# Optimization experiments

Hardware: AMD Instinct MI355X
Metric: run time of the kernel (lower is better)

## Reference

```python
import jax, jax.numpy as jnp
import numpy as np

B, N, C_IN = 4, 4096, 64
DIM = 64
NKP = 15
K = 32               # neighbor_limits
CONV_RADIUS = 0.1 * 2.0   # conv_radius * rigid_scale (is_deform=False)
KERNEL_RADIUS = 0.12
RECEP = 1.2          # kernel_point_receptive_radius
TRANS_DIM = 128
INF = 1000000.0


def _square_distance(src, dst):
    # src [B,N,3], dst [B,M,3] -> [B,N,M]
    d = -2.0 * jnp.einsum('bnc,bmc->bnm', src, dst)
    d = d + jnp.sum(src * src, -1)[:, :, None]
    d = d + jnp.sum(dst * dst, -1)[:, None, :]
    return d


def _query_ball(xyz, radius):
    # xyz [B,N,3] -> neighbor idx [B,N,K]; out-of-radius mapped to N (shadow)
    n = xyz.shape[1]
    sq = _square_distance(xyz, xyz)
    idx = jnp.broadcast_to(jnp.arange(n, dtype=jnp.int32), sq.shape)
    idx = jnp.where(sq > radius * radius, n, idx)
    idx = jnp.sort(idx, axis=-1)[:, :, :K]
    return idx


def _index_points(points_bcn, idx, pad_val):
    # points [B,C,N], idx [B,N,K] -> [B,N,K,C]; index N hits shadow row = pad_val
    p = jnp.transpose(points_bcn, (0, 2, 1))          # [B,N,C]
    shadow = jnp.full((p.shape[0], 1, p.shape[2]), pad_val, p.dtype)
    p = jnp.concatenate([p, shadow], axis=1)          # [B,N+1,C]
    b_idx = jnp.arange(p.shape[0])[:, None, None]
    return p[b_idx, idx]                              # [B,N,K,C]


def setup_inputs() -> dict:
    key = jax.random.key(0)
    ks = jax.random.split(key, 12)
    pos = jax.random.uniform(ks[0], (B, 3, N), dtype=jnp.float32)
    feat = jax.random.normal(ks[1], (B, C_IN, N), dtype=jnp.float32)
    # kernel points: center point at origin, rest inside kernel_radius ball ('center' mode)
    kp_rest = jax.random.uniform(ks[2], (3, NKP - 1), minval=-KERNEL_RADIUS,
                                 maxval=KERNEL_RADIUS, dtype=jnp.float32)
    kp_pos = jnp.concatenate([jnp.zeros((3, 1), jnp.float32), kp_rest], axis=1)  # [3,NKP]
    s = 0.05
    cb_w = jax.random.normal(ks[3], (DIM, C_IN), jnp.float32) * s
    cb_b = jax.random.normal(ks[4], (DIM,), jnp.float32) * s
    kp_weight = jax.random.normal(ks[5], (NKP, DIM, DIM), jnp.float32) * s
    kp_bias = jax.random.normal(ks[6], (DIM,), jnp.float32) * s
    ce_w = jax.random.normal(ks[7], (C_IN, DIM), jnp.float32) * s
    ce_b = jax.random.normal(ks[8], (C_IN,), jnp.float32) * s
    f1_w = jax.random.normal(ks[9], (2 * DIM, 2 * DIM), jnp.float32) * s
    f1_b = jnp.zeros((2 * DIM,), jnp.float32)
    f2_w = jax.random.normal(ks[10], (TRANS_DIM, 2 * DIM), jnp.float32) * s
    f2_b = jnp.zeros((TRANS_DIM,), jnp.float32)
    return dict(pos=pos, feat=feat, kp_pos=kp_pos, cb_w=cb_w, cb_b=cb_b,
                kp_weight=kp_weight, kp_bias=kp_bias, ce_w=ce_w, ce_b=ce_b,
                f1_w=f1_w, f1_b=f1_b, f2_w=f2_w, f2_b=f2_b)


def reference(pos, feat, kp_pos, cb_w, cb_b, kp_weight, kp_bias, ce_w, ce_b,
              f1_w, f1_b, f2_w, f2_b):
    xyz = jnp.transpose(jax.lax.stop_gradient(pos), (0, 2, 1))       # [B,N,3]
    neighbor_idx = _query_ball(xyz, CONV_RADIUS)                     # [B,N,K]
    # NOTE: with is_deform=False the original code does NOT subtract the center
    # position; rel_neighbor_pos is the absolute gathered positions.
    neighbor_pos = jnp.transpose(_index_points(pos, neighbor_idx, INF),
                                 (0, 3, 1, 2))                        # [B,3,N,K]
    feat0 = jnp.einsum('oc,bcn->bon', cb_w, feat) + cb_b[None, :, None]
    neighbor_feat = _index_points(feat0, neighbor_idx, 0.0)           # [B,N,K,DIM]

    kp_pos_deform = kp_pos.reshape(1, 3, 1, NKP) + 0.0                # offset = 0
    diff = neighbor_pos[..., None] - kp_pos_deform[:, :, :, None, :]  # [B,3,N,K,NKP]
    sq_d = jnp.sum(diff * diff, axis=1)                               # [B,N,K,NKP]
    w = jnp.clip(1.0 - jnp.sqrt(sq_d) / RECEP, 0.0)                   # [B,N,K,NKP]
    w = jnp.transpose(w, (0, 1, 3, 2))                                # [B,N,NKP,K]
    weighted = jnp.einsum('bnpk,bnkc->bnpc', w, neighbor_feat)        # [B,N,NKP,DIM]
    out = jnp.einsum('bnpc,pcd->bnd', weighted, kp_weight) + kp_bias  # [B,N,DIM]
    out = jax.nn.relu(jnp.transpose(out, (0, 2, 1)))                  # [B,DIM,N]
    out = jax.nn.relu(jnp.einsum('oc,bcn->bon', ce_w, out)
                      + ce_b[None, :, None] + feat)                   # [B,C_IN,N]

    fuse_in = jnp.concatenate(
        [jnp.transpose(weighted, (0, 3, 1, 2)),                       # [B,DIM,N,NKP]
         jnp.broadcast_to(out[..., None], (B, DIM, N, NKP))], axis=1) # [B,2DIM,N,NKP]
    h = jax.nn.relu(jnp.einsum('oc,bcnk->bonk', f1_w, fuse_in)
                    + f1_b[None, :, None, None])
    fuse = jax.nn.relu(jnp.einsum('oc,bcnk->bonk', f2_w, h)
                       + f2_b[None, :, None, None])                   # [B,TRANS_DIM,N,NKP]
    return out, kp_pos_deform, fuse
```

## Files before the change

kernel.cpp:

```cpp
#include <hip/hip_runtime.h>
#include <hip/hip_bf16.h>
#include <stdint.h>

#define NPTS 4096
#define NB   4
#define KNN  32
#define NKPT 15

#define OFF_IDX      0ULL
#define OFF_FEAT0    2097152ULL
#define OFF_WEIGHTED 6292480ULL
#define OFF_HO       37749760ULL
#define OFF_W1P      46138368ULL
#define OFF_W2P      46171136ULL
#define OFF_KPWP     46203904ULL

#define OUT_OFF_OUT  0
#define OUT_OFF_KP   1048576
#define OUT_OFF_FUSE 1048621

#define SBU(u) ((u) ^ (((u) >> 3) & 7))

typedef __attribute__((ext_vector_type(8))) short short8v;
typedef __attribute__((ext_vector_type(4))) float f32x4;

__device__ __forceinline__ unsigned short bf16b(float f) {
  __hip_bfloat16 h = __float2bfloat16(f);
  return *(unsigned short*)&h;
}
__device__ __forceinline__ unsigned pkbf(float lo, float hi) {
  return (unsigned)bf16b(lo) | ((unsigned)bf16b(hi) << 16);
}

__global__ __launch_bounds__(256) void k012(const float* __restrict__ pos,
                                            const float* __restrict__ feat,
                                            const float* __restrict__ cb_w,
                                            const float* __restrict__ cb_b,
                                            const float* __restrict__ f1_w,
                                            const float* __restrict__ f2_w,
                                            const float* __restrict__ kpw,
                                            const float* __restrict__ kp_pos,
                                            int* __restrict__ idx_ws,
                                            float* __restrict__ feat0,
                                            unsigned short* __restrict__ w1p,
                                            unsigned short* __restrict__ w2p,
                                            unsigned short* __restrict__ kpwp,
                                            float* __restrict__ out_kp) {
  __shared__ float cbt[64 * 65];
  const int blk = blockIdx.x;
  if (blk < 4096) {
    const int w = threadIdx.x >> 6, lane = threadIdx.x & 63;
    const int pt = blk * 4 + w;
    const int b = pt >> 12, n = pt & 4095;
    const float* px = pos + (size_t)b * 3 * NPTS;
    const double x0 = (double)px[n], y0 = (double)px[NPTS + n], z0 = (double)px[2 * NPTS + n];
    const double ssrc = x0 * x0 + y0 * y0 + z0 * z0;
    const double RAD = 0.1 * 2.0;
    const double R2 = RAD * RAD;
    int cnt = 0;
    int* op = idx_ws + (size_t)pt * KNN;
    for (int ch = 0; ch < 64; ++ch) {
      const int j = ch * 64 + lane;
      const double xj = (double)px[j], yj = (double)px[NPTS + j], zj = (double)px[2 * NPTS + j];
      const double dot  = x0 * xj + y0 * yj + z0 * zj;
      const double sdst = xj * xj + yj * yj + zj * zj;
      const double sq = -2.0 * dot + ssrc + sdst;
      const bool keep = !(sq > R2);
      const unsigned long long m = __ballot(keep);
      if (keep) {
        const int p = cnt + (int)__popcll(m & ((1ULL << lane) - 1ULL));
        if (p < KNN) op[p] = j;
      }
      cnt += (int)__popcll(m);
      if (cnt >= KNN) break;
    }
    const int s = cnt + lane;
    if (s < KNN) op[s] = NPTS;
    return;
  }
  if (blk < 8192) {
    const int t = threadIdx.x;
    #pragma unroll
    for (int q = 0; q < 16; ++q) {
      const int idx = q * 256 + t;
      const int d = idx >> 6, c = idx & 63;
      cbt[c * 65 + d] = cb_w[idx];
    }
    __syncthreads();
    const int ptl = t >> 6, d = t & 63;
    const int pt = (blk - 4096) * 4 + ptl;
    const int b = pt >> 12, n = pt & 4095;
    const float* fp = feat + (size_t)b * 64 * NPTS + n;
    float acc = 0.f;
    #pragma unroll
    for (int c = 0; c < 64; ++c) acc = fmaf(cbt[c * 65 + d], fp[(size_t)c * NPTS], acc);
    acc += cb_b[d];
    feat0[((size_t)b * (NPTS + 1) + n) * 64 + d] = acc;
    return;
  }
  int t = (blk - 8192) * 256 + threadIdx.x;
  if (t < 32768) {
    const int w = t >> 14;
    const int i = t & 16383;
    const int j = i & 7, l = (i >> 3) & 63, kc = (i >> 9) & 3, ot = i >> 11;
    const int o = ot * 16 + (l & 15);
    const int k = kc * 32 + (l >> 4) * 8 + j;
    const float* src = w ? f2_w : f1_w;
    unsigned short* dst = w ? w2p : w1p;
    dst[i] = bf16b(src[o * 128 + k]);
    return;
  }
  t -= 32768;
  if (t < 61440) {
    const int j = t & 7, l = (t >> 3) & 63, nt = (t >> 9) & 3, kc = t >> 11;
    const int k = kc * 32 + (l >> 4) * 8 + j;
    const int d = nt * 16 + (l & 15);
    kpwp[t] = bf16b(kpw[(size_t)k * 64 + d]);
    return;
  }
  t -= 61440;
  if (t < NB * 64) { int b = t >> 6, d = t & 63; feat0[((size_t)b * (NPTS + 1) + NPTS) * 64 + d] = 0.f; return; }
  t -= NB * 64;
  if (t < 45) out_kp[t] = kp_pos[t];
}

__global__ __launch_bounds__(64) void k3_weighted(const float* __restrict__ pos,
                                                  const int* __restrict__ idx_ws,
                                                  const float* __restrict__ feat0,
                                                  const float* __restrict__ kp_pos,
                                                  unsigned short* __restrict__ wbf) {
  __shared__ int   nidx[KNN];
  __shared__ float npx[KNN], npy[KNN], npz[KNN];
  __shared__ float kp[48];
  __shared__ float wl[KNN * 16];
  const int lane = threadIdx.x;
  const int pt = blockIdx.x;
  const int b = pt >> 12;
  if (lane < 45) kp[lane] = kp_pos[lane];
  if (lane < KNN) {
    const int ki = idx_ws[(size_t)pt * KNN + lane];
    nidx[lane] = ki;
    const bool v = ki < NPTS;
    const float* px = pos + (size_t)b * 3 * NPTS;
    npx[lane] = v ? px[ki] : 1000000.0f;
    npy[lane] = v ? px[NPTS + ki] : 1000000.0f;
    npz[lane] = v ? px[2 * NPTS + ki] : 1000000.0f;
  }
  __syncthreads();
  #pragma unroll
  for (int r = 0; r < 8; ++r) {
    const int i = r * 64 + lane;
    const int k = i >> 4, p = i & 15;
    float wv = 0.f;
    if (p < 15) {
      const float dx = npx[k] - kp[p];
      const float dy = npy[k] - kp[15 + p];
      const float dz = npz[k] - kp[30 + p];
      const float d2 = dx * dx + dy * dy + dz * dz;
      wv = fmaxf(1.0f - sqrtf(d2) / 1.2f, 0.f);
    }
    wl[i] = wv;
  }
  __syncthreads();
  float acc[16];
  #pragma unroll
  for (int p = 0; p < 16; ++p) acc[p] = 0.f;
  const float* f0 = feat0 + (size_t)b * (NPTS + 1) * 64 + lane;
  for (int k = 0; k < KNN; ++k) {
    const float f = f0[(size_t)nidx[k] * 64];
    #pragma unroll
    for (int q = 0; q < 4; ++q) {
      const float4 w4 = *(const float4*)&wl[k * 16 + q * 4];
      acc[q * 4 + 0] = fmaf(w4.x, f, acc[q * 4 + 0]);
      acc[q * 4 + 1] = fmaf(w4.y, f, acc[q * 4 + 1]);
      acc[q * 4 + 2] = fmaf(w4.z, f, acc[q * 4 + 2]);
      acc[q * 4 + 3] = fmaf(w4.w, f, acc[q * 4 + 3]);
    }
  }
  unsigned short* wp = wbf + (size_t)pt * NKPT * 64 + lane;
  #pragma unroll
  for (int p = 0; p < 15; ++p) wp[(size_t)p * 64] = bf16b(acc[p]);
}

__global__ __launch_bounds__(256) void k45(const unsigned short* __restrict__ wbf,
                                           const unsigned short* __restrict__ kpwp,
                                           const float* __restrict__ kp_bias,
                                           const float* __restrict__ ce_w,
                                           const float* __restrict__ ce_b,
                                           const float* __restrict__ feat,
                                           const unsigned short* __restrict__ w1p,
                                           const float* __restrict__ f1_b,
                                           float* __restrict__ out,
                                           float* __restrict__ hO) {
  __shared__ float r0[64 * 65];
  __shared__ float cwt[64 * 64];
  __shared__ unsigned short outT[64 * 74];
  const int t = threadIdx.x;
  const int b = blockIdx.x >> 6;
  const int n0 = (blockIdx.x & 63) * 64;
  const int wv = t >> 6, lane = t & 63;
  #pragma unroll
  for (int q = 0; q < 16; ++q) {
    const int idx = q * 256 + t;
    cwt[idx] = ce_w[(idx & 63) * 64 + (idx >> 6)];
  }
  const short8v* kf = (const short8v*)kpwp;
  f32x4 acc[4];
  #pragma unroll
  for (int nt = 0; nt < 4; ++nt) acc[nt] = (f32x4){0.f, 0.f, 0.f, 0.f};
  const int m0 = b * 4096 + n0 + wv * 16;
  const unsigned short* ap = wbf + (size_t)(m0 + (lane & 15)) * 960 + (lane >> 4) * 8;
  #pragma unroll 6
  for (int kc = 0; kc < 30; ++kc) {
    const short8v a = *(const short8v*)&ap[kc * 32];
    #pragma unroll
    for (int nt = 0; nt < 4; ++nt)
      acc[nt] = __builtin_amdgcn_mfma_f32_16x16x32_bf16(a, kf[(kc * 4 + nt) * 64 + lane], acc[nt], 0, 0, 0);
  }
  const int rl = wv * 16 + (lane >> 4) * 4;
  #pragma unroll
  for (int nt = 0; nt < 4; ++nt) {
    const int d = nt * 16 + (lane & 15);
    const float bv = kp_bias[d];
    #pragma unroll
    for (int r = 0; r < 4; ++r)
      r0[(rl + r) * 65 + d] = fmaxf(acc[nt][r] + bv, 0.f);
  }
  __syncthreads();
  const int nl = t & 63, og = t >> 6;
  float facc[16];
  #pragma unroll
  for (int j = 0; j < 16; ++j) facc[j] = 0.f;
  for (int c = 0; c < 64; ++c) {
    const float x = r0[nl * 65 + c];
    #pragma unroll
    for (int q = 0; q < 4; ++q) {
      const float4 w4 = *(const float4*)&cwt[c * 64 + og * 16 + q * 4];
      facc[q * 4 + 0] = fmaf(w4.x, x, facc[q * 4 + 0]);
      facc[q * 4 + 1] = fmaf(w4.y, x, facc[q * 4 + 1]);
      facc[q * 4 + 2] = fmaf(w4.z, x, facc[q * 4 + 2]);
      facc[q * 4 + 3] = fmaf(w4.w, x, facc[q * 4 + 3]);
    }
  }
  #pragma unroll
  for (int q = 0; q < 4; ++q) {
    const float4 cb4 = *(const float4*)&ce_b[og * 16 + q * 4];
    const float cbv[4] = {cb4.x, cb4.y, cb4.z, cb4.w};
    #pragma unroll
    for (int j = 0; j < 4; ++j) {
      const int o = og * 16 + q * 4 + j;
      const float fv = feat[((size_t)b * 64 + o) * 4096 + n0 + nl];
      const float v = fmaxf((facc[q * 4 + j] + cbv[j]) + fv, 0.f);
      out[((size_t)b * 64 + o) * 4096 + n0 + nl] = v;
      outT[o * 74 + nl] = bf16b(v);
    }
  }
  __syncthreads();
  const short8v* w1f = (const short8v*)w1p;
  f32x4 hacc[8];
  #pragma unroll
  for (int ot = 0; ot < 8; ++ot) hacc[ot] = (f32x4){0.f, 0.f, 0.f, 0.f};
  const int nw = lane & 15;
  #pragma unroll
  for (int kc2 = 0; kc2 < 2; ++kc2) {
    short8v bfr;
    #pragma unroll
    for (int j = 0; j < 8; ++j)
      bfr[j] = (short)outT[(kc2 * 32 + (lane >> 4) * 8 + j) * 74 + wv * 16 + nw];
    #pragma unroll
    for (int ot = 0; ot < 8; ++ot)
      hacc[ot] = __builtin_amdgcn_mfma_f32_16x16x32_bf16(w1f[(ot * 4 + 2 + kc2) * 64 + lane], bfr, hacc[ot], 0, 0, 0);
  }
  const int rb = (lane >> 4) * 4;
  float* hp = hO + ((size_t)b * 4096 + n0 + wv * 16 + nw) * 128;
  #pragma unroll
  for (int ot = 0; ot < 8; ++ot) {
    const float4 b1 = *(const float4*)&f1_b[ot * 16 + rb];
    const float bv[4] = {b1.x, b1.y, b1.z, b1.w};
    #pragma unroll
    for (int r = 0; r < 4; ++r)
      hp[ot * 16 + rb + r] = hacc[ot][r] + bv[r];
  }
}

__global__ __launch_bounds__(256, 2) void k6_fuse(const unsigned short* __restrict__ wbf,
                                                  const float* __restrict__ hO,
                                                  const unsigned short* __restrict__ w1p,
                                                  const unsigned short* __restrict__ w2p,
                                                  const float* __restrict__ f2_b,
                                                  float* __restrict__ fuse) {
  __shared__ __attribute__((aligned(16))) unsigned short SB[16384];
  __shared__ __attribute__((aligned(16))) float hOS[12 * 128];
  const int t = threadIdx.x;
  const int blk = blockIdx.x;
  const int b = blk / 480;
  const int ml0 = (blk - b * 480) * 128;
  const size_t M0 = (size_t)blk * 128;
  const int wv = t >> 6, lane = t & 63;
  const short8v* w1f = (const short8v*)w1p;
  const short8v* w2f = (const short8v*)w2p;

  short8v w1r[16];
  #pragma unroll
  for (int ot = 0; ot < 8; ++ot)
    #pragma unroll
    for (int kc = 0; kc < 2; ++kc)
      w1r[ot * 2 + kc] = w1f[(ot * 4 + kc) * 64 + lane];

  #pragma unroll
  for (int q = 0; q < 4; ++q) {
    const int chunk = q * 256 + t;
    const int m = chunk >> 3, a = chunk & 7;
    const uint4 pk = *(const uint4*)&wbf[(M0 + m) * 64 + a * 8];
    const int kc = a >> 2, hi = a & 3;
    const int u = ((m >> 4) * 4 + kc) * 64 + hi * 16 + (m & 15);
    *(uint4*)&SB[SBU(u) * 8] = pk;
  }
  const int nmin = ml0 / 15;
  #pragma unroll
  for (int q = 0; q < 6; ++q) {
    const int idx = q * 256 + t;
    const int row = idx >> 7, o = idx & 127;
    int n = nmin + row;
    if (n > 4095) n = 4095;
    hOS[idx] = hO[((size_t)b * 4096 + n) * 128 + o];
  }
  __syncthreads();

  short8v xf[4];
  #pragma unroll
  for (int mt = 0; mt < 2; ++mt)
    #pragma unroll
    for (int kc = 0; kc < 2; ++kc) {
      const int u = ((wv * 2 + mt) * 4 + kc) * 64 + lane;
      xf[mt * 2 + kc] = *(const short8v*)&SB[SBU(u) * 8];
    }

  const int rb = (lane >> 4) * 4;
  const int dnA = (ml0 + wv * 32 + (lane & 15)) / 15 - nmin;
  const int dnB = (ml0 + wv * 32 + 16 + (lane & 15)) / 15 - nmin;
  f32x4 acc[8][2];
  #pragma unroll
  for (int ot = 0; ot < 8; ++ot) {
    acc[ot][0] = *(const f32x4*)&hOS[dnA * 128 + ot * 16 + rb];
    acc[ot][1] = *(const f32x4*)&hOS[dnB * 128 + ot * 16 + rb];
  }
  #pragma unroll
  for (int kc = 0; kc < 2; ++kc) {
    #pragma unroll
    for (int ot = 0; ot < 8; ++ot) {
      acc[ot][0] = __builtin_amdgcn_mfma_f32_16x16x32_bf16(w1r[ot * 2 + kc], xf[kc],     acc[ot][0], 0, 0, 0);
      acc[ot][1] = __builtin_amdgcn_mfma_f32_16x16x32_bf16(w1r[ot * 2 + kc], xf[2 + kc], acc[ot][1], 0, 0, 0);
    }
  }
  short8v w2r[32];
  #pragma unroll
  for (int i = 0; i < 32; ++i) w2r[i] = w2f[i * 64 + lane];

  #pragma unroll
  for (int ot = 0; ot < 8; ++ot) {
    const int o0 = ot * 16 + rb;
    const int kc = o0 >> 5, hi = (o0 >> 3) & 3, j0 = o0 & 7;
    #pragma unroll
    for (int mt = 0; mt < 2; ++mt) {
      const f32x4 h = acc[ot][mt];
      const float h0 = fmaxf(h[0], 0.f);
      const float h1 = fmaxf(h[1], 0.f);
      const float h2 = fmaxf(h[2], 0.f);
      const float h3 = fmaxf(h[3], 0.f);
      const int u = ((wv * 2 + mt) * 4 + kc) * 64 + hi * 16 + (lane & 15);
      uint2 pk;
      pk.x = pkbf(h0, h1);
      pk.y = pkbf(h2, h3);
      *(uint2*)&SB[SBU(u) * 8 + j0] = pk;
    }
  }
  short8v hf[8];
  #pragma unroll
  for (int mt = 0; mt < 2; ++mt)
    #pragma unroll
    for (int kc = 0; kc < 4; ++kc) {
      const int u = ((wv * 2 + mt) * 4 + kc) * 64 + lane;
      hf[mt * 4 + kc] = *(const short8v*)&SB[SBU(u) * 8];
    }
  #pragma unroll
  for (int ot = 0; ot < 8; ++ot) {
    acc[ot][0] = (f32x4){0.f, 0.f, 0.f, 0.f};
    acc[ot][1] = (f32x4){0.f, 0.f, 0.f, 0.f};
  }
  #pragma unroll
  for (int kc = 0; kc < 4; ++kc) {
    #pragma unroll
    for (int ot = 0; ot < 8; ++ot) {
      acc[ot][0] = __builtin_amdgcn_mfma_f32_16x16x32_bf16(w2r[ot * 4 + kc], hf[kc],     acc[ot][0], 0, 0, 0);
      acc[ot][1] = __builtin_amdgcn_mfma_f32_16x16x32_bf16(w2r[ot * 4 + kc], hf[4 + kc], acc[ot][1], 0, 0, 0);
    }
  }
  float* fp0 = fuse + (size_t)b * 128 * 61440 + ml0 + wv * 32 + (lane & 15);
  #pragma unroll
  for (int ot = 0; ot < 8; ++ot) {
    const int o0 = ot * 16 + rb;
    const float4 b2 = *(const float4*)&f2_b[o0];
    const float bv[4] = {b2.x, b2.y, b2.z, b2.w};
    #pragma unroll
    for (int mt = 0; mt < 2; ++mt) {
      const f32x4 vacc = acc[ot][mt];
      #pragma unroll
      for (int r = 0; r < 4; ++r)
        fp0[(size_t)(o0 + r) * 61440 + mt * 16] = fmaxf(vacc[r] + bv[r], 0.f);
    }
  }
}

extern "C" void kernel_launch(void* const* d_in, const int* in_sizes, int n_in,
                              void* d_out, int out_size, void* d_ws, size_t ws_size,
                              hipStream_t stream) {
  const float* pos     = (const float*)d_in[0];
  const float* feat    = (const float*)d_in[1];
  const float* kp_pos  = (const float*)d_in[2];
  const float* cb_w    = (const float*)d_in[3];
  const float* cb_b    = (const float*)d_in[4];
  const float* kpw     = (const float*)d_in[5];
  const float* kp_bias = (const float*)d_in[6];
  const float* ce_w    = (const float*)d_in[7];
  const float* ce_b    = (const float*)d_in[8];
  const float* f1_w    = (const float*)d_in[9];
  const float* f1_b    = (const float*)d_in[10];
  const float* f2_w    = (const float*)d_in[11];
  const float* f2_b    = (const float*)d_in[12];
  float* out = (float*)d_out;
  char* ws = (char*)d_ws;
  int*   idx_ws   = (int*)(ws + OFF_IDX);
  float* feat0    = (float*)(ws + OFF_FEAT0);
  unsigned short* wbf  = (unsigned short*)(ws + OFF_WEIGHTED);
  float* hO       = (float*)(ws + OFF_HO);
  unsigned short* w1p  = (unsigned short*)(ws + OFF_W1P);
  unsigned short* w2p  = (unsigned short*)(ws + OFF_W2P);
  unsigned short* kpwp = (unsigned short*)(ws + OFF_KPWP);

  k012<<<8562, 256, 0, stream>>>(pos, feat, cb_w, cb_b, f1_w, f2_w, kpw, kp_pos,
                                 idx_ws, feat0, w1p, w2p, kpwp, out + OUT_OFF_KP);
  k3_weighted<<<16384, 64, 0, stream>>>(pos, idx_ws, feat0, kp_pos, wbf);
  k45<<<256, 256, 0, stream>>>(wbf, kpwp, kp_bias, ce_w, ce_b, feat, w1p, f1_b,
                               out + OUT_OFF_OUT, hO);
  k6_fuse<<<1920, 256, 0, stream>>>(wbf, hO, w1p, w2p, f2_b, out + OUT_OFF_FUSE);
}
```

Before: 134.2 us.

## Stage fuse output through LDS for coalesced stores; pack four points per k3 block

The fuse kernel's epilogue now writes MFMA accumulators into shared memory in 32-row chunks and then stores full 128-column rows to global memory, so stores to the large fuse output are contiguous instead of scattered 16-wide fragments. This adds barriers and LDS traffic per chunk. Separately, k3_weighted now processes four points per 256-thread block instead of one point per 64-thread block, cutting block count and per-block overhead.

```diff
diff --git a/kernel.cpp b/kernel.cpp
--- a/kernel.cpp
+++ b/kernel.cpp
@@ -124,42 +124,42 @@
   if (t < 45) out_kp[t] = kp_pos[t];
 }
 
-__global__ __launch_bounds__(64) void k3_weighted(const float* __restrict__ pos,
-                                                  const int* __restrict__ idx_ws,
-                                                  const float* __restrict__ feat0,
-                                                  const float* __restrict__ kp_pos,
-                                                  unsigned short* __restrict__ wbf) {
-  __shared__ int   nidx[KNN];
-  __shared__ float npx[KNN], npy[KNN], npz[KNN];
+__global__ __launch_bounds__(256) void k3_weighted(const float* __restrict__ pos,
+                                                   const int* __restrict__ idx_ws,
+                                                   const float* __restrict__ feat0,
+                                                   const float* __restrict__ kp_pos,
+                                                   unsigned short* __restrict__ wbf) {
+  __shared__ int   nidx[4][KNN];
+  __shared__ float npx[4][KNN], npy[4][KNN], npz[4][KNN];
   __shared__ float kp[48];
-  __shared__ float wl[KNN * 16];
-  const int lane = threadIdx.x;
-  const int pt = blockIdx.x;
+  __shared__ float wl[4][KNN * 16];
+  const int wv = threadIdx.x >> 6, lane = threadIdx.x & 63;
+  const int pt = blockIdx.x * 4 + wv;
   const int b = pt >> 12;
-  if (lane < 45) kp[lane] = kp_pos[lane];
+  if (threadIdx.x < 45) kp[threadIdx.x] = kp_pos[threadIdx.x];
   if (lane < KNN) {
     const int ki = idx_ws[(size_t)pt * KNN + lane];
-    nidx[lane] = ki;
+    nidx[wv][lane] = ki;
     const bool v = ki < NPTS;
     const float* px = pos + (size_t)b * 3 * NPTS;
-    npx[lane] = v ? px[ki] : 1000000.0f;
-    npy[lane] = v ? px[NPTS + ki] : 1000000.0f;
-    npz[lane] = v ? px[2 * NPTS + ki] : 1000000.0f;
+    npx[wv][lane] = v ? px[ki] : 1000000.0f;
+    npy[wv][lane] = v ? px[NPTS + ki] : 1000000.0f;
+    npz[wv][lane] = v ? px[2 * NPTS + ki] : 1000000.0f;
   }
   __syncthreads();
   #pragma unroll
   for (int r = 0; r < 8; ++r) {
     const int i = r * 64 + lane;
     const int k = i >> 4, p = i & 15;
-    float wv = 0.f;
+    float wvv = 0.f;
     if (p < 15) {
-      const float dx = npx[k] - kp[p];
-      const float dy = npy[k] - kp[15 + p];
-      const float dz = npz[k] - kp[30 + p];
+      const float dx = npx[wv][k] - kp[p];
+      const float dy = npy[wv][k] - kp[15 + p];
+      const float dz = npz[wv][k] - kp[30 + p];
       const float d2 = dx * dx + dy * dy + dz * dz;
-      wv = fmaxf(1.0f - sqrtf(d2) / 1.2f, 0.f);
-    }
-    wl[i] = wv;
+      wvv = fmaxf(1.0f - sqrtf(d2) / 1.2f, 0.f);
+    }
+    wl[wv][i] = wvv;
   }
   __syncthreads();
   float acc[16];
@@ -167,10 +167,10 @@
   for (int p = 0; p < 16; ++p) acc[p] = 0.f;
   const float* f0 = feat0 + (size_t)b * (NPTS + 1) * 64 + lane;
   for (int k = 0; k < KNN; ++k) {
-    const float f = f0[(size_t)nidx[k] * 64];
+    const float f = f0[(size_t)nidx[wv][k] * 64];
     #pragma unroll
     for (int q = 0; q < 4; ++q) {
-      const float4 w4 = *(const float4*)&wl[k * 16 + q * 4];
+      const float4 w4 = *(const float4*)&wl[wv][k * 16 + q * 4];
       acc[q * 4 + 0] = fmaf(w4.x, f, acc[q * 4 + 0]);
       acc[q * 4 + 1] = fmaf(w4.y, f, acc[q * 4 + 1]);
       acc[q * 4 + 2] = fmaf(w4.z, f, acc[q * 4 + 2]);
@@ -383,6 +383,7 @@
       const int u = ((wv * 2 + mt) * 4 + kc) * 64 + lane;
       hf[mt * 4 + kc] = *(const short8v*)&SB[SBU(u) * 8];
     }
+  __syncthreads();
   #pragma unroll
   for (int ot = 0; ot < 8; ++ot) {
     acc[ot][0] = (f32x4){0.f, 0.f, 0.f, 0.f};
@@ -396,19 +397,33 @@
       acc[ot][1] = __builtin_amdgcn_mfma_f32_16x16x32_bf16(w2r[ot * 4 + kc], hf[4 + kc], acc[ot][1], 0, 0, 0);
     }
   }
-  float* fp0 = fuse + (size_t)b * 128 * 61440 + ml0 + wv * 32 + (lane & 15);
-  #pragma unroll
-  for (int ot = 0; ot < 8; ++ot) {
-    const int o0 = ot * 16 + rb;
-    const float4 b2 = *(const float4*)&f2_b[o0];
-    const float bv[4] = {b2.x, b2.y, b2.z, b2.w};
-    #pragma unroll
-    for (int mt = 0; mt < 2; ++mt) {
-      const f32x4 vacc = acc[ot][mt];
+  float* SBf = (float*)SB;
+  const int colw = wv * 32 + (lane & 15);
+  float* fblk = fuse + (size_t)b * 128 * 61440 + ml0;
+  #pragma unroll
+  for (int p = 0; p < 4; ++p) {
+    #pragma unroll
+    for (int oi = 0; oi < 2; ++oi) {
+      const int ot = p * 2 + oi;
+      const int o0 = ot * 16 + rb;
+      const float4 b2 = *(const float4*)&f2_b[o0];
+      const float bv[4] = {b2.x, b2.y, b2.z, b2.w};
       #pragma unroll
-      for (int r = 0; r < 4; ++r)
-        fp0[(size_t)(o0 + r) * 61440 + mt * 16] = fmaxf(vacc[r] + bv[r], 0.f);
-    }
+      for (int mt = 0; mt < 2; ++mt) {
+        const f32x4 v = acc[ot][mt];
+        #pragma unroll
+        for (int r = 0; r < 4; ++r)
+          SBf[(oi * 16 + rb + r) * 132 + colw + mt * 16] = fmaxf(v[r] + bv[r], 0.f);
+      }
+    }
+    __syncthreads();
+    #pragma unroll
+    for (int q = 0; q < 16; ++q) {
+      const int idx = q * 256 + t;
+      const int row = idx >> 7, c = idx & 127;
+      fblk[(size_t)(p * 32 + row) * 61440 + c] = SBf[row * 132 + c];
+    }
+    __syncthreads();
   }
 }
 
@@ -440,7 +455,7 @@
 
   k012<<<8562, 256, 0, stream>>>(pos, feat, cb_w, cb_b, f1_w, f2_w, kpw, kp_pos,
                                  idx_ws, feat0, w1p, w2p, kpwp, out + OUT_OFF_KP);
-  k3_weighted<<<16384, 64, 0, stream>>>(pos, idx_ws, feat0, kp_pos, wbf);
+  k3_weighted<<<4096, 256, 0, stream>>>(pos, idx_ws, feat0, kp_pos, wbf);
   k45<<<256, 256, 0, stream>>>(wbf, kpwp, kp_bias, ce_w, ce_b, feat, w1p, f1_b,
                                out + OUT_OFF_OUT, hO);
   k6_fuse<<<1920, 256, 0, stream>>>(wbf, hO, w1p, w2p, f2_b, out + OUT_OFF_FUSE);
```

After: 137.3 us. +2.3%, slower.
